# Performance work log

Measured on AMD Instinct MI355X. Metric: run time of the kernel, lower is better.

Reference implementation:

```python
import jax, jax.numpy as jnp
import numpy as np

EPS = 1e-5
D_MODEL, D_INNER, D_STATE, DT_RANK, K = 2048, 4096, 16, 128, 4

def setup_inputs() -> dict:
    key = jax.random.key(0)
    ks = jax.random.split(key, 13)
    B = 128
    s = lambda k, shape, sc=0.02: jax.random.normal(k, shape, jnp.float32) * sc
    return {
        "hidden_states": jax.random.normal(ks[0], (B, 1, D_MODEL), jnp.float32),
        "conv_state": jax.random.normal(ks[1], (B, D_INNER, K - 1), jnp.float32),
        "ssm_state": jax.random.normal(ks[2], (B, D_INNER, D_STATE), jnp.float32),
        "norm_w": jnp.ones((D_MODEL,), jnp.float32),
        "in_proj_w": s(ks[3], (2 * D_INNER, D_MODEL)),           # no bias (HF Mamba default)
        "conv_w": s(ks[4], (D_INNER, K), 0.1),                    # depthwise conv kernel
        "conv_b": s(ks[5], (D_INNER,), 0.1),
        "x_proj_w": s(ks[6], (DT_RANK + 2 * D_STATE, D_INNER)),
        "dt_proj_w": s(ks[7], (D_INNER, DT_RANK)),
        "dt_proj_b": s(ks[8], (D_INNER,), 0.1),
        "A_log": jnp.log(jnp.broadcast_to(jnp.arange(1, D_STATE + 1, dtype=jnp.float32), (D_INNER, D_STATE))),
        "D": jnp.ones((D_INNER,), jnp.float32),
        "out_proj_w": s(ks[9], (D_MODEL, D_INNER)),               # no bias
    }

def reference(hidden_states, conv_state, ssm_state, norm_w, in_proj_w, conv_w, conv_b,
              x_proj_w, dt_proj_w, dt_proj_b, A_log, D, out_proj_w):
    x = hidden_states[:, 0, :]                                   # (B, d_model)
    # RMSNorm (pre-norm)
    normed = x * jax.lax.rsqrt(jnp.mean(x * x, axis=-1, keepdims=True) + EPS) * norm_w
    # in_proj -> gate z and conv branch xc
    xz = normed @ in_proj_w.T                                    # (B, 2*d_inner)
    xc, z = jnp.split(xz, 2, axis=-1)
    # depthwise causal conv, single-step with rolling cache
    conv_in = jnp.concatenate([conv_state, xc[:, :, None]], axis=-1)  # (B, d_inner, K)
    new_conv_state = conv_in[:, :, 1:]
    xact = jax.nn.silu(jnp.sum(conv_in * conv_w[None], axis=-1) + conv_b)  # (B, d_inner)
    # input-dependent SSM params
    proj = xact @ x_proj_w.T                                     # (B, dt_rank + 2*d_state)
    dt_raw = proj[:, :DT_RANK]
    Bmat = proj[:, DT_RANK:DT_RANK + D_STATE]                    # (B, d_state)
    Cmat = proj[:, DT_RANK + D_STATE:]                           # (B, d_state)
    dt = jax.nn.softplus(dt_raw @ dt_proj_w.T + dt_proj_b)       # (B, d_inner)
    A = -jnp.exp(A_log)                                          # (d_inner, d_state)
    dA = jnp.exp(dt[:, :, None] * A[None])                       # (B, d_inner, d_state)
    dB = dt[:, :, None] * Bmat[:, None, :]
    new_ssm_state = ssm_state * dA + dB * xact[:, :, None]
    y = jnp.sum(new_ssm_state * Cmat[:, None, :], axis=-1) + D * xact
    y = y * jax.nn.silu(z)
    out = y @ out_proj_w.T                                       # (B, d_model)
    output = out[:, None, :] + hidden_states                     # residual add
    return output, new_conv_state, new_ssm_state
```

## Files before the change

kernel.cpp:

```cpp
#include <hip/hip_runtime.h>

typedef __attribute__((ext_vector_type(8))) short bf16x8;
typedef __attribute__((ext_vector_type(4))) float f32x4;
typedef __attribute__((ext_vector_type(8))) unsigned short u16x8;
typedef __attribute__((ext_vector_type(4))) unsigned short u16x4;
typedef __attribute__((ext_vector_type(2))) unsigned u32x2;

#define DM 2048
#define DI 4096
#define BATCH 128

__device__ __forceinline__ unsigned short f2bf(float f) {
  union { float f; unsigned u; } v; v.f = f;
  unsigned r = v.u + 0x7FFFu + ((v.u >> 16) & 1u);
  return (unsigned short)(r >> 16);
}
__device__ __forceinline__ float bf2f(unsigned short u) {
  union { unsigned u; float f; } v; v.u = (unsigned)u << 16; return v.f;
}
__device__ __forceinline__ unsigned pk2bf(float lo, float hi) {
  unsigned r;
  asm("v_cvt_pk_bf16_f32 %0, %1, %2" : "=v"(r) : "v"(lo), "v"(hi));
  return r;
}
__device__ __forceinline__ float sigm(float x) { return 1.f / (1.f + __expf(-x)); }

constexpr int BK = 64;
constexpr int LDT = BK + 8;

#define LDREGS(AR, ARF, BR, kb_) do {                                                     \
    int kb = (kb_);                                                                       \
    if constexpr (ABF) {                                                                  \
      _Pragma("unroll") for (int i = 0; i < BM / 32; ++i) {                               \
        int idx = tid + i * 256, r = idx >> 3, c = (idx & 7) * 8;                         \
        AR[i] = *(const u16x8*)&((const unsigned short*)Ag)[(long)(m0 + r) * lda + kb + c]; \
      }                                                                                   \
    } else {                                                                              \
      _Pragma("unroll") for (int i = 0; i < BM / 16; ++i) {                               \
        int idx = tid + i * 256, r = idx >> 4, c = (idx & 15) * 4;                        \
        ARF[i] = *(const f32x4*)&((const float*)Ag)[(long)(m0 + r) * lda + kb + c];       \
      }                                                                                   \
    }                                                                                     \
    _Pragma("unroll") for (int i = 0; i < BN / 16; ++i) {                                 \
      int idx = tid + i * 256, r = idx >> 4, c = (idx & 15) * 4;                          \
      BR[i] = *(const f32x4*)&Bg[(long)(n0 + r) * ldb + kb + c];                          \
    }                                                                                     \
  } while (0)

#define STLDS(AR, ARF, BR, buf_) do {                                                     \
    unsigned short* As_ = lds + (buf_) * BUF;                                             \
    unsigned short* Bs_ = As_ + BM * LDT;                                                 \
    if constexpr (ABF) {                                                                  \
      _Pragma("unroll") for (int i = 0; i < BM / 32; ++i) {                               \
        int idx = tid + i * 256, r = idx >> 3, c = (idx & 7) * 8;                         \
        *(u16x8*)&As_[r * LDT + c] = AR[i];                                               \
      }                                                                                   \
    } else {                                                                              \
      _Pragma("unroll") for (int i = 0; i < BM / 16; ++i) {                               \
        int idx = tid + i * 256, r = idx >> 4, c = (idx & 15) * 4;                        \
        u32x2 o; o[0] = pk2bf(ARF[i][0], ARF[i][1]); o[1] = pk2bf(ARF[i][2], ARF[i][3]); \
        *(u32x2*)&As_[r * LDT + c] = o;                                                   \
      }                                                                                   \
    }                                                                                     \
    _Pragma("unroll") for (int i = 0; i < BN / 16; ++i) {                                 \
      int idx = tid + i * 256, r = idx >> 4, c = (idx & 15) * 4;                          \
      u32x2 o; o[0] = pk2bf(BR[i][0], BR[i][1]); o[1] = pk2bf(BR[i][2], BR[i][3]);       \
      *(u32x2*)&Bs_[r * LDT + c] = o;                                                     \
    }                                                                                     \
  } while (0)

#define COMPUTE(buf_) do {                                                                \
    const unsigned short* As_ = lds + (buf_) * BUF;                                       \
    const unsigned short* Bs_ = As_ + BM * LDT;                                           \
    _Pragma("unroll") for (int kk = 0; kk < BK; kk += 32) {                               \
      int kr = kk + lhi * 8;                                                              \
      bf16x8 af[MI], bfr[NF];                                                             \
      _Pragma("unroll") for (int mi = 0; mi < MI; ++mi)                                   \
        af[mi] = *(const bf16x8*)&As_[(wm * (BM / 2) + mi * 16 + llo) * LDT + kr];        \
      _Pragma("unroll") for (int ni = 0; ni < NF; ++ni)                                   \
        bfr[ni] = *(const bf16x8*)&Bs_[(wn * 16 * NF + ni * 16 + llo) * LDT + kr];        \
      _Pragma("unroll") for (int mi = 0; mi < MI; ++mi)                                   \
        _Pragma("unroll") for (int ni = 0; ni < NF; ++ni)                                 \
          acc[mi * NF + ni] = __builtin_amdgcn_mfma_f32_16x16x32_bf16(                    \
              af[mi], bfr[ni], acc[mi * NF + ni], 0, 0, 0);                               \
    }                                                                                     \
  } while (0)

template<int BM, int BN, bool ABF>
__device__ __forceinline__ void gemmMN(const void* Ag, int lda, const float* Bg, int ldb,
                                       int m0, int n0, int k0, int k1, unsigned short* lds,
                                       f32x4* acc) {
  constexpr int NF = BN / 32;
  constexpr int MI = BM / 32;
  constexpr int BUF = (BM + BN) * LDT;
  const int tid = threadIdx.x, lane = tid & 63, wave = tid >> 6;
  const int wm = wave >> 1, wn = wave & 1, llo = lane & 15, lhi = lane >> 4;

  u16x8 ar0[ABF ? BM / 32 : 1], ar1[ABF ? BM / 32 : 1];
  f32x4 arf0[ABF ? 1 : BM / 16], arf1[ABF ? 1 : BM / 16];
  f32x4 br0[BN / 16], br1[BN / 16];

  const int nt = (k1 - k0) / BK;
  LDREGS(ar0, arf0, br0, k0);
  LDREGS(ar1, arf1, br1, k0 + BK);
  STLDS(ar0, arf0, br0, 0);
  __syncthreads();
  int t = 0;
  while (true) {
    if (t + 2 < nt) LDREGS(ar0, arf0, br0, k0 + (t + 2) * BK);
    COMPUTE(0);
    if (t + 1 < nt) STLDS(ar1, arf1, br1, 1);
    __syncthreads();
    if (++t == nt) break;
    if (t + 2 < nt) LDREGS(ar1, arf1, br1, k0 + (t + 2) * BK);
    COMPUTE(1);
    if (t + 1 < nt) STLDS(ar0, arf0, br0, 0);
    __syncthreads();
    if (++t == nt) break;
  }
}

__global__ __launch_bounds__(256) void k01_prep(const float* __restrict__ hs,
                                                const float* __restrict__ nw,
                                                unsigned short* __restrict__ normed,
                                                float* __restrict__ outp,
                                                float* __restrict__ xz,
                                                float* __restrict__ proj) {
  int blk = blockIdx.x, tid = threadIdx.x;
  int t = blk * 256 + tid;
  f32x4 z = {};
  *(f32x4*)&xz[t * 4] = z;
  if (t < 65536) *(f32x4*)&outp[t * 4] = *(const f32x4*)&hs[t * 4];
  if (t < 5120) *(f32x4*)&proj[t * 4] = z;
  if (blk < 128) {
    int b = blk;
    const float* xr = hs + (long)b * DM;
    f32x4 v0 = *(const f32x4*)&xr[tid * 4];
    f32x4 v1 = *(const f32x4*)&xr[(tid + 256) * 4];
    float ss = v0[0]*v0[0] + v0[1]*v0[1] + v0[2]*v0[2] + v0[3]*v0[3]
             + v1[0]*v1[0] + v1[1]*v1[1] + v1[2]*v1[2] + v1[3]*v1[3];
    for (int off = 32; off; off >>= 1) ss += __shfl_xor(ss, off);
    __shared__ float red[4];
    if ((tid & 63) == 0) red[tid >> 6] = ss;
    __syncthreads();
    ss = red[0] + red[1] + red[2] + red[3];
    float rstd = rsqrtf(ss * (1.f / DM) + 1e-5f);
    f32x4 w0 = *(const f32x4*)&nw[tid * 4];
    f32x4 w1 = *(const f32x4*)&nw[(tid + 256) * 4];
    u32x2 o0, o1;
    o0[0] = pk2bf(v0[0] * rstd * w0[0], v0[1] * rstd * w0[1]);
    o0[1] = pk2bf(v0[2] * rstd * w0[2], v0[3] * rstd * w0[3]);
    o1[0] = pk2bf(v1[0] * rstd * w1[0], v1[1] * rstd * w1[1]);
    o1[1] = pk2bf(v1[2] * rstd * w1[2], v1[3] * rstd * w1[3]);
    *(u32x2*)&normed[(long)b * DM + tid * 4] = o0;
    *(u32x2*)&normed[(long)b * DM + (tid + 256) * 4] = o1;
  }
}

__global__ __launch_bounds__(256) void k2_inproj(const unsigned short* __restrict__ normed,
                                                 const float* __restrict__ W,
                                                 float* __restrict__ xz) {
  __shared__ unsigned short lds[2 * (128 + 64) * LDT];
  f32x4 acc[8] = {};
  int bn = blockIdx.x, sk = blockIdx.y;
  gemmMN<128, 64, true>(normed, DM, W, DM, 0, bn * 64, sk * 512, sk * 512 + 512, lds, acc);
  int tid = threadIdx.x, lane = tid & 63, wave = tid >> 6, wm = wave >> 1, wn = wave & 1;
  int llo = lane & 15, lhi = lane >> 4;
#pragma unroll
  for (int mi = 0; mi < 4; ++mi)
#pragma unroll
    for (int ni = 0; ni < 2; ++ni)
#pragma unroll
      for (int r = 0; r < 4; ++r) {
        int b = wm * 64 + mi * 16 + lhi * 4 + r;
        int n = bn * 64 + wn * 32 + ni * 16 + llo;
        atomicAdd(&xz[(long)b * 8192 + n], acc[mi * 2 + ni][r]);
      }
}

__global__ __launch_bounds__(256) void e2_conv(const float* __restrict__ xz,
                                               const float* __restrict__ conv_state,
                                               const float* __restrict__ conv_w,
                                               const float* __restrict__ conv_b,
                                               float* __restrict__ out_ncs,
                                               float* __restrict__ xact_f,
                                               unsigned short* __restrict__ xact_b,
                                               unsigned short* __restrict__ szb) {
  int p = blockIdx.x * 256 + threadIdx.x;
  int b = p >> 12, n = p & 4095;
  float xc = xz[(long)b * 8192 + n];
  float z  = xz[(long)b * 8192 + DI + n];
  const float* cs = conv_state + (long)p * 3;
  float c0 = cs[0], c1 = cs[1], c2 = cs[2];
  f32x4 cw = *(const f32x4*)&conv_w[n * 4];
  float xs = c0 * cw[0] + c1 * cw[1] + c2 * cw[2] + xc * cw[3] + conv_b[n];
  float xa = xs * sigm(xs);
  float* ncs = out_ncs + (long)p * 3;
  ncs[0] = c1; ncs[1] = c2; ncs[2] = xc;
  xact_f[p] = xa;
  xact_b[p] = f2bf(xa);
  szb[p] = f2bf(z * sigm(z));
}

__global__ __launch_bounds__(256) void k3_xproj(const unsigned short* __restrict__ xact_b,
                                                const float* __restrict__ XW,
                                                float* __restrict__ proj) {
  __shared__ unsigned short lds[2 * (128 + 32) * LDT];
  f32x4 acc[4] = {};
  int bn = blockIdx.x, kc = blockIdx.y;
  gemmMN<128, 32, true>(xact_b, DI, XW, DI, 0, bn * 32, kc * 128, kc * 128 + 128, lds, acc);
  int tid = threadIdx.x, lane = tid & 63, wave = tid >> 6, wm = wave >> 1, wn = wave & 1;
  int llo = lane & 15, lhi = lane >> 4;
  int n = bn * 32 + wn * 16 + llo;
#pragma unroll
  for (int mi = 0; mi < 4; ++mi)
#pragma unroll
    for (int r = 0; r < 4; ++r) {
      int b = wm * 64 + mi * 16 + lhi * 4 + r;
      atomicAdd(&proj[b * 160 + n], acc[mi][r]);
    }
}

__global__ __launch_bounds__(256) void k45_dtssm(const float* __restrict__ proj,
                                                 const float* __restrict__ DW,
                                                 const float* __restrict__ dtb,
                                                 const float* __restrict__ A_log,
                                                 const float* __restrict__ Dp,
                                                 const float* __restrict__ ssm,
                                                 const float* __restrict__ xact_f,
                                                 const unsigned short* __restrict__ szb,
                                                 float* __restrict__ out_nss,
                                                 unsigned short* __restrict__ yz_b) {
  __shared__ unsigned short lds[2 * (32 + 32) * LDT];
  f32x4 acc[1] = {};
  int nb = blockIdx.x, mb = blockIdx.y;
  gemmMN<32, 32, false>(proj, 160, DW, 128, mb * 32, nb * 32, 0, 128, lds, acc);
  int tid = threadIdx.x, lane = tid & 63, wave = tid >> 6, wm = wave >> 1, wn = wave & 1;
  int llo = lane & 15, lhi = lane >> 4;
  int n = nb * 32 + wn * 16 + llo;
  float dtbn = dtb[n], Dn = Dp[n];
  f32x4 Al0 = *(const f32x4*)&A_log[n * 16];
  f32x4 Al1 = *(const f32x4*)&A_log[n * 16 + 4];
  f32x4 Al2 = *(const f32x4*)&A_log[n * 16 + 8];
  f32x4 Al3 = *(const f32x4*)&A_log[n * 16 + 12];
  float aS[16];
#pragma unroll
  for (int j = 0; j < 4; ++j) {
    aS[j] = -__expf(Al0[j]); aS[4 + j] = -__expf(Al1[j]);
    aS[8 + j] = -__expf(Al2[j]); aS[12 + j] = -__expf(Al3[j]);
  }
#pragma unroll
  for (int r = 0; r < 4; ++r) {
    int b = mb * 32 + wm * 16 + lhi * 4 + r;
    long p = (long)b * DI + n;
    float v = acc[0][r] + dtbn;
    float dtv = (v > 20.f) ? v : log1pf(__expf(v));
    float xa = xact_f[p];
    const float* Bp = proj + b * 160 + 128;
    const float* Cp = proj + b * 160 + 144;
    const float* sp = ssm + p * 16;
    float* np = out_nss + p * 16;
    float y = 0.f;
#pragma unroll
    for (int q = 0; q < 4; ++q) {
      f32x4 sv = *(const f32x4*)&sp[q * 4];
      f32x4 Bv = *(const f32x4*)&Bp[q * 4];
      f32x4 Cv = *(const f32x4*)&Cp[q * 4];
      f32x4 nv;
#pragma unroll
      for (int j = 0; j < 4; ++j) {
        float dA = __expf(dtv * aS[q * 4 + j]);
        nv[j] = sv[j] * dA + dtv * Bv[j] * xa;
        y += nv[j] * Cv[j];
      }
      *(f32x4*)&np[q * 4] = nv;
    }
    yz_b[p] = f2bf((y + Dn * xa) * bf2f(szb[p]));
  }
}

__global__ __launch_bounds__(256) void k5_outproj(const unsigned short* __restrict__ yz_b,
                                                  const float* __restrict__ OW,
                                                  float* __restrict__ outp) {
  __shared__ unsigned short lds[2 * (128 + 32) * LDT];
  f32x4 acc[4] = {};
  int bn = blockIdx.x, sk = blockIdx.y;
  gemmMN<128, 32, true>(yz_b, DI, OW, DI, 0, bn * 32, sk * 512, sk * 512 + 512, lds, acc);
  int tid = threadIdx.x, lane = tid & 63, wave = tid >> 6, wm = wave >> 1, wn = wave & 1;
  int llo = lane & 15, lhi = lane >> 4;
  int n = bn * 32 + wn * 16 + llo;
#pragma unroll
  for (int mi = 0; mi < 4; ++mi)
#pragma unroll
    for (int r = 0; r < 4; ++r) {
      int b = wm * 64 + mi * 16 + lhi * 4 + r;
      atomicAdd(&outp[(long)b * DM + n], acc[mi][r]);
    }
}

extern "C" void kernel_launch(void* const* d_in, const int* in_sizes, int n_in, void* d_out,
                              int out_size, void* d_ws, size_t ws_size, hipStream_t stream) {
  const float* hs         = (const float*)d_in[0];
  const float* conv_state = (const float*)d_in[1];
  const float* ssm        = (const float*)d_in[2];
  const float* norm_w     = (const float*)d_in[3];
  const float* in_proj_w  = (const float*)d_in[4];
  const float* conv_w     = (const float*)d_in[5];
  const float* conv_b     = (const float*)d_in[6];
  const float* x_proj_w   = (const float*)d_in[7];
  const float* dt_proj_w  = (const float*)d_in[8];
  const float* dt_proj_b  = (const float*)d_in[9];
  const float* A_log      = (const float*)d_in[10];
  const float* Dp         = (const float*)d_in[11];
  const float* out_proj_w = (const float*)d_in[12];

  float* outp    = (float*)d_out;
  float* out_ncs = outp + 262144;
  float* out_nss = outp + 262144 + 1572864;

  char* ws = (char*)d_ws;
  unsigned short* normed = (unsigned short*)(ws);
  float*          xz     = (float*)(ws + 2097152);
  unsigned short* yz_b   = (unsigned short*)(ws + 2097152);
  float*          xact_f = (float*)(ws + 6291456);
  unsigned short* xact_b = (unsigned short*)(ws + 8388608);
  unsigned short* szb    = (unsigned short*)(ws + 9437184);
  float*          proj   = (float*)(ws + 10485760);

  hipLaunchKernelGGL(k01_prep, dim3(1024), dim3(256), 0, stream, hs, norm_w, normed, outp, xz, proj);
  hipLaunchKernelGGL(k2_inproj, dim3(128, 4), dim3(256), 0, stream, normed, in_proj_w, xz);
  hipLaunchKernelGGL(e2_conv, dim3(2048), dim3(256), 0, stream, xz, conv_state, conv_w, conv_b,
                     out_ncs, xact_f, xact_b, szb);
  hipLaunchKernelGGL(k3_xproj, dim3(5, 32), dim3(256), 0, stream, xact_b, x_proj_w, proj);
  hipLaunchKernelGGL(k45_dtssm, dim3(128, 4), dim3(256), 0, stream, proj, dt_proj_w, dt_proj_b,
                     A_log, Dp, ssm, xact_f, szb, out_nss, yz_b);
  hipLaunchKernelGGL(k5_outproj, dim3(64, 8), dim3(256), 0, stream, yz_b, out_proj_w, outp);
}
```

Baseline: 77.72 us.

## Stream fp32 weights directly into MFMA registers with LDS-resident activation tile

```diff
diff --git a/kernel.cpp b/kernel.cpp
--- a/kernel.cpp
+++ b/kernel.cpp
@@ -5,6 +5,7 @@
 typedef __attribute__((ext_vector_type(8))) unsigned short u16x8;
 typedef __attribute__((ext_vector_type(4))) unsigned short u16x4;
 typedef __attribute__((ext_vector_type(2))) unsigned u32x2;
+typedef __attribute__((ext_vector_type(4))) unsigned u32x4u;
 
 #define DM 2048
 #define DI 4096
@@ -24,6 +25,49 @@
   return r;
 }
 __device__ __forceinline__ float sigm(float x) { return 1.f / (1.f + __expf(-x)); }
+
+__device__ __forceinline__ void stream_gemm(const unsigned short* __restrict__ Ab, long lda,
+                                            const float* __restrict__ Bg, long ldb,
+                                            int n0, int k0, unsigned short* As, f32x4* acc) {
+  const int tid = threadIdx.x, lane = tid & 63, wave = tid >> 6;
+  const int wm = wave >> 1, wn = wave & 1, llo = lane & 15, lhi = lane >> 4;
+#pragma unroll
+  for (int i = 0; i < 32; ++i) {
+    int idx = tid + i * 256;
+    int r = idx >> 6, c8 = (idx & 63) * 8;
+    int kb = c8 * 2;
+    *(u16x8*)&((char*)As)[r * 1024 + (kb ^ ((r & 7) << 4))] =
+        *(const u16x8*)&Ab[(long)r * lda + k0 + c8];
+  }
+  __syncthreads();
+#pragma unroll
+  for (int kk = 0; kk < 512; kk += 32) {
+    bf16x8 af[4], bfr[2];
+#pragma unroll
+    for (int mi = 0; mi < 4; ++mi) {
+      int row = wm * 64 + mi * 16 + llo;
+      int kb = (kk + lhi * 8) * 2;
+      af[mi] = *(const bf16x8*)&((const char*)As)[row * 1024 + (kb ^ ((row & 7) << 4))];
+    }
+#pragma unroll
+    for (int ni = 0; ni < 2; ++ni) {
+      long n = n0 + wn * 32 + ni * 16 + llo;
+      const float* bp = &Bg[n * ldb + k0 + kk + lhi * 8];
+      f32x4 b0 = *(const f32x4*)bp;
+      f32x4 b1 = *(const f32x4*)(bp + 4);
+      union { u32x4u u; bf16x8 h; } cv;
+      cv.u[0] = pk2bf(b0[0], b0[1]); cv.u[1] = pk2bf(b0[2], b0[3]);
+      cv.u[2] = pk2bf(b1[0], b1[1]); cv.u[3] = pk2bf(b1[2], b1[3]);
+      bfr[ni] = cv.h;
+    }
+#pragma unroll
+    for (int mi = 0; mi < 4; ++mi)
+#pragma unroll
+      for (int ni = 0; ni < 2; ++ni)
+        acc[mi * 2 + ni] =
+            __builtin_amdgcn_mfma_f32_16x16x32_bf16(af[mi], bfr[ni], acc[mi * 2 + ni], 0, 0, 0);
+  }
+}
 
 constexpr int BK = 64;
 constexpr int LDT = BK + 8;
@@ -157,13 +201,13 @@
   }
 }
 
-__global__ __launch_bounds__(256) void k2_inproj(const unsigned short* __restrict__ normed,
-                                                 const float* __restrict__ W,
-                                                 float* __restrict__ xz) {
-  __shared__ unsigned short lds[2 * (128 + 64) * LDT];
+__global__ __launch_bounds__(256) void k2s_inproj(const unsigned short* __restrict__ normed,
+                                                  const float* __restrict__ W,
+                                                  float* __restrict__ xz) {
+  __shared__ unsigned short As[128 * 512];
   f32x4 acc[8] = {};
   int bn = blockIdx.x, sk = blockIdx.y;
-  gemmMN<128, 64, true>(normed, DM, W, DM, 0, bn * 64, sk * 512, sk * 512 + 512, lds, acc);
+  stream_gemm(normed, DM, W, DM, bn * 64, sk * 512, As, acc);
   int tid = threadIdx.x, lane = tid & 63, wave = tid >> 6, wm = wave >> 1, wn = wave & 1;
   int llo = lane & 15, lhi = lane >> 4;
 #pragma unroll
@@ -279,23 +323,25 @@
   }
 }
 
-__global__ __launch_bounds__(256) void k5_outproj(const unsigned short* __restrict__ yz_b,
-                                                  const float* __restrict__ OW,
-                                                  float* __restrict__ outp) {
-  __shared__ unsigned short lds[2 * (128 + 32) * LDT];
-  f32x4 acc[4] = {};
+__global__ __launch_bounds__(256) void k5s_outproj(const unsigned short* __restrict__ yz_b,
+                                                   const float* __restrict__ OW,
+                                                   float* __restrict__ outp) {
+  __shared__ unsigned short As[128 * 512];
+  f32x4 acc[8] = {};
   int bn = blockIdx.x, sk = blockIdx.y;
-  gemmMN<128, 32, true>(yz_b, DI, OW, DI, 0, bn * 32, sk * 512, sk * 512 + 512, lds, acc);
+  stream_gemm(yz_b, DI, OW, DI, bn * 64, sk * 512, As, acc);
   int tid = threadIdx.x, lane = tid & 63, wave = tid >> 6, wm = wave >> 1, wn = wave & 1;
   int llo = lane & 15, lhi = lane >> 4;
-  int n = bn * 32 + wn * 16 + llo;
 #pragma unroll
   for (int mi = 0; mi < 4; ++mi)
 #pragma unroll
-    for (int r = 0; r < 4; ++r) {
-      int b = wm * 64 + mi * 16 + lhi * 4 + r;
-      atomicAdd(&outp[(long)b * DM + n], acc[mi][r]);
-    }
+    for (int ni = 0; ni < 2; ++ni)
+#pragma unroll
+      for (int r = 0; r < 4; ++r) {
+        int b = wm * 64 + mi * 16 + lhi * 4 + r;
+        int n = bn * 64 + wn * 32 + ni * 16 + llo;
+        atomicAdd(&outp[(long)b * DM + n], acc[mi * 2 + ni][r]);
+      }
 }
 
 extern "C" void kernel_launch(void* const* d_in, const int* in_sizes, int n_in, void* d_out,
@@ -328,11 +374,11 @@
   float*          proj   = (float*)(ws + 10485760);
 
   hipLaunchKernelGGL(k01_prep, dim3(1024), dim3(256), 0, stream, hs, norm_w, normed, outp, xz, proj);
-  hipLaunchKernelGGL(k2_inproj, dim3(128, 4), dim3(256), 0, stream, normed, in_proj_w, xz);
+  hipLaunchKernelGGL(k2s_inproj, dim3(128, 4), dim3(256), 0, stream, normed, in_proj_w, xz);
   hipLaunchKernelGGL(e2_conv, dim3(2048), dim3(256), 0, stream, xz, conv_state, conv_w, conv_b,
                      out_ncs, xact_f, xact_b, szb);
   hipLaunchKernelGGL(k3_xproj, dim3(5, 32), dim3(256), 0, stream, xact_b, x_proj_w, proj);
   hipLaunchKernelGGL(k45_dtssm, dim3(128, 4), dim3(256), 0, stream, proj, dt_proj_w, dt_proj_b,
                      A_log, Dp, ssm, xact_f, szb, out_nss, yz_b);
-  hipLaunchKernelGGL(k5_outproj, dim3(64, 8), dim3(256), 0, stream, yz_b, out_proj_w, outp);
-}
+  hipLaunchKernelGGL(k5s_outproj, dim3(32, 8), dim3(256), 0, stream, yz_b, out_proj_w, outp);
+}
```

Result: slower. 97.60 us (+25.6%).

## Replace split-K atomic accumulation with partial buffers and explicit reduction passes

Applied to the files above, without the earlier changes.

```diff
diff --git a/kernel.cpp b/kernel.cpp
--- a/kernel.cpp
+++ b/kernel.cpp
@@ -3,7 +3,6 @@
 typedef __attribute__((ext_vector_type(8))) short bf16x8;
 typedef __attribute__((ext_vector_type(4))) float f32x4;
 typedef __attribute__((ext_vector_type(8))) unsigned short u16x8;
-typedef __attribute__((ext_vector_type(4))) unsigned short u16x4;
 typedef __attribute__((ext_vector_type(2))) unsigned u32x2;
 
 #define DM 2048
@@ -120,52 +119,42 @@
   }
 }
 
-__global__ __launch_bounds__(256) void k01_prep(const float* __restrict__ hs,
-                                                const float* __restrict__ nw,
-                                                unsigned short* __restrict__ normed,
-                                                float* __restrict__ outp,
-                                                float* __restrict__ xz,
-                                                float* __restrict__ proj) {
-  int blk = blockIdx.x, tid = threadIdx.x;
-  int t = blk * 256 + tid;
-  f32x4 z = {};
-  *(f32x4*)&xz[t * 4] = z;
-  if (t < 65536) *(f32x4*)&outp[t * 4] = *(const f32x4*)&hs[t * 4];
-  if (t < 5120) *(f32x4*)&proj[t * 4] = z;
-  if (blk < 128) {
-    int b = blk;
-    const float* xr = hs + (long)b * DM;
-    f32x4 v0 = *(const f32x4*)&xr[tid * 4];
-    f32x4 v1 = *(const f32x4*)&xr[(tid + 256) * 4];
-    float ss = v0[0]*v0[0] + v0[1]*v0[1] + v0[2]*v0[2] + v0[3]*v0[3]
-             + v1[0]*v1[0] + v1[1]*v1[1] + v1[2]*v1[2] + v1[3]*v1[3];
-    for (int off = 32; off; off >>= 1) ss += __shfl_xor(ss, off);
-    __shared__ float red[4];
-    if ((tid & 63) == 0) red[tid >> 6] = ss;
-    __syncthreads();
-    ss = red[0] + red[1] + red[2] + red[3];
-    float rstd = rsqrtf(ss * (1.f / DM) + 1e-5f);
-    f32x4 w0 = *(const f32x4*)&nw[tid * 4];
-    f32x4 w1 = *(const f32x4*)&nw[(tid + 256) * 4];
-    u32x2 o0, o1;
-    o0[0] = pk2bf(v0[0] * rstd * w0[0], v0[1] * rstd * w0[1]);
-    o0[1] = pk2bf(v0[2] * rstd * w0[2], v0[3] * rstd * w0[3]);
-    o1[0] = pk2bf(v1[0] * rstd * w1[0], v1[1] * rstd * w1[1]);
-    o1[1] = pk2bf(v1[2] * rstd * w1[2], v1[3] * rstd * w1[3]);
-    *(u32x2*)&normed[(long)b * DM + tid * 4] = o0;
-    *(u32x2*)&normed[(long)b * DM + (tid + 256) * 4] = o1;
-  }
+__global__ __launch_bounds__(256) void k1_rmsnorm(const float* __restrict__ hs,
+                                                  const float* __restrict__ nw,
+                                                  unsigned short* __restrict__ normed) {
+  int b = blockIdx.x, tid = threadIdx.x;
+  const float* xr = hs + (long)b * DM;
+  f32x4 v0 = *(const f32x4*)&xr[tid * 4];
+  f32x4 v1 = *(const f32x4*)&xr[(tid + 256) * 4];
+  float ss = v0[0]*v0[0] + v0[1]*v0[1] + v0[2]*v0[2] + v0[3]*v0[3]
+           + v1[0]*v1[0] + v1[1]*v1[1] + v1[2]*v1[2] + v1[3]*v1[3];
+  for (int off = 32; off; off >>= 1) ss += __shfl_xor(ss, off);
+  __shared__ float red[4];
+  if ((tid & 63) == 0) red[tid >> 6] = ss;
+  __syncthreads();
+  ss = red[0] + red[1] + red[2] + red[3];
+  float rstd = rsqrtf(ss * (1.f / DM) + 1e-5f);
+  f32x4 w0 = *(const f32x4*)&nw[tid * 4];
+  f32x4 w1 = *(const f32x4*)&nw[(tid + 256) * 4];
+  u32x2 o0, o1;
+  o0[0] = pk2bf(v0[0] * rstd * w0[0], v0[1] * rstd * w0[1]);
+  o0[1] = pk2bf(v0[2] * rstd * w0[2], v0[3] * rstd * w0[3]);
+  o1[0] = pk2bf(v1[0] * rstd * w1[0], v1[1] * rstd * w1[1]);
+  o1[1] = pk2bf(v1[2] * rstd * w1[2], v1[3] * rstd * w1[3]);
+  *(u32x2*)&normed[(long)b * DM + tid * 4] = o0;
+  *(u32x2*)&normed[(long)b * DM + (tid + 256) * 4] = o1;
 }
 
 __global__ __launch_bounds__(256) void k2_inproj(const unsigned short* __restrict__ normed,
                                                  const float* __restrict__ W,
-                                                 float* __restrict__ xz) {
+                                                 float* __restrict__ xzp) {
   __shared__ unsigned short lds[2 * (128 + 64) * LDT];
   f32x4 acc[8] = {};
   int bn = blockIdx.x, sk = blockIdx.y;
   gemmMN<128, 64, true>(normed, DM, W, DM, 0, bn * 64, sk * 512, sk * 512 + 512, lds, acc);
   int tid = threadIdx.x, lane = tid & 63, wave = tid >> 6, wm = wave >> 1, wn = wave & 1;
   int llo = lane & 15, lhi = lane >> 4;
+  float* dst = xzp + (long)sk * (BATCH * 8192);
 #pragma unroll
   for (int mi = 0; mi < 4; ++mi)
 #pragma unroll
@@ -174,11 +163,11 @@
       for (int r = 0; r < 4; ++r) {
         int b = wm * 64 + mi * 16 + lhi * 4 + r;
         int n = bn * 64 + wn * 32 + ni * 16 + llo;
-        atomicAdd(&xz[(long)b * 8192 + n], acc[mi * 2 + ni][r]);
+        dst[(long)b * 8192 + n] = acc[mi * 2 + ni][r];
       }
 }
 
-__global__ __launch_bounds__(256) void e2_conv(const float* __restrict__ xz,
+__global__ __launch_bounds__(256) void e2_conv(const float* __restrict__ xzp,
                                                const float* __restrict__ conv_state,
                                                const float* __restrict__ conv_w,
                                                const float* __restrict__ conv_b,
@@ -188,8 +177,13 @@
                                                unsigned short* __restrict__ szb) {
   int p = blockIdx.x * 256 + threadIdx.x;
   int b = p >> 12, n = p & 4095;
-  float xc = xz[(long)b * 8192 + n];
-  float z  = xz[(long)b * 8192 + DI + n];
+  long base = (long)b * 8192 + n;
+  float xc = 0.f, z = 0.f;
+#pragma unroll
+  for (int s = 0; s < 4; ++s) {
+    xc += xzp[(long)s * (BATCH * 8192) + base];
+    z  += xzp[(long)s * (BATCH * 8192) + base + DI];
+  }
   const float* cs = conv_state + (long)p * 3;
   float c0 = cs[0], c1 = cs[1], c2 = cs[2];
   f32x4 cw = *(const f32x4*)&conv_w[n * 4];
@@ -204,7 +198,7 @@
 
 __global__ __launch_bounds__(256) void k3_xproj(const unsigned short* __restrict__ xact_b,
                                                 const float* __restrict__ XW,
-                                                float* __restrict__ proj) {
+                                                float* __restrict__ projp) {
   __shared__ unsigned short lds[2 * (128 + 32) * LDT];
   f32x4 acc[4] = {};
   int bn = blockIdx.x, kc = blockIdx.y;
@@ -212,13 +206,26 @@
   int tid = threadIdx.x, lane = tid & 63, wave = tid >> 6, wm = wave >> 1, wn = wave & 1;
   int llo = lane & 15, lhi = lane >> 4;
   int n = bn * 32 + wn * 16 + llo;
+  float* dst = projp + (long)kc * (BATCH * 160);
 #pragma unroll
   for (int mi = 0; mi < 4; ++mi)
 #pragma unroll
     for (int r = 0; r < 4; ++r) {
       int b = wm * 64 + mi * 16 + lhi * 4 + r;
-      atomicAdd(&proj[b * 160 + n], acc[mi][r]);
+      dst[b * 160 + n] = acc[mi][r];
     }
+}
+
+__global__ __launch_bounds__(256) void k3r_reduce(const float* __restrict__ projp,
+                                                  float* __restrict__ proj) {
+  int t = blockIdx.x * 256 + threadIdx.x;
+  f32x4 s = {};
+#pragma unroll
+  for (int k = 0; k < 32; ++k) {
+    f32x4 v = *(const f32x4*)&projp[(long)k * (BATCH * 160) + t * 4];
+    s[0] += v[0]; s[1] += v[1]; s[2] += v[2]; s[3] += v[3];
+  }
+  *(f32x4*)&proj[t * 4] = s;
 }
 
 __global__ __launch_bounds__(256) void k45_dtssm(const float* __restrict__ proj,
@@ -281,7 +288,7 @@
 
 __global__ __launch_bounds__(256) void k5_outproj(const unsigned short* __restrict__ yz_b,
                                                   const float* __restrict__ OW,
-                                                  float* __restrict__ outp) {
+                                                  float* __restrict__ op) {
   __shared__ unsigned short lds[2 * (128 + 32) * LDT];
   f32x4 acc[4] = {};
   int bn = blockIdx.x, sk = blockIdx.y;
@@ -289,13 +296,27 @@
   int tid = threadIdx.x, lane = tid & 63, wave = tid >> 6, wm = wave >> 1, wn = wave & 1;
   int llo = lane & 15, lhi = lane >> 4;
   int n = bn * 32 + wn * 16 + llo;
+  float* dst = op + (long)sk * (BATCH * DM);
 #pragma unroll
   for (int mi = 0; mi < 4; ++mi)
 #pragma unroll
     for (int r = 0; r < 4; ++r) {
       int b = wm * 64 + mi * 16 + lhi * 4 + r;
-      atomicAdd(&outp[(long)b * DM + n], acc[mi][r]);
+      dst[(long)b * DM + n] = acc[mi][r];
     }
+}
+
+__global__ __launch_bounds__(256) void k7_out(const float* __restrict__ op,
+                                              const float* __restrict__ hs,
+                                              float* __restrict__ outp) {
+  int t = blockIdx.x * 256 + threadIdx.x;
+  f32x4 s = *(const f32x4*)&hs[t * 4];
+#pragma unroll
+  for (int k = 0; k < 8; ++k) {
+    f32x4 v = *(const f32x4*)&op[(long)k * (BATCH * DM) + t * 4];
+    s[0] += v[0]; s[1] += v[1]; s[2] += v[2]; s[3] += v[3];
+  }
+  *(f32x4*)&outp[t * 4] = s;
 }
 
 extern "C" void kernel_launch(void* const* d_in, const int* in_sizes, int n_in, void* d_out,
@@ -320,19 +341,23 @@
 
   char* ws = (char*)d_ws;
   unsigned short* normed = (unsigned short*)(ws);
-  float*          xz     = (float*)(ws + 2097152);
-  unsigned short* yz_b   = (unsigned short*)(ws + 2097152);
-  float*          xact_f = (float*)(ws + 6291456);
-  unsigned short* xact_b = (unsigned short*)(ws + 8388608);
-  unsigned short* szb    = (unsigned short*)(ws + 9437184);
-  float*          proj   = (float*)(ws + 10485760);
-
-  hipLaunchKernelGGL(k01_prep, dim3(1024), dim3(256), 0, stream, hs, norm_w, normed, outp, xz, proj);
-  hipLaunchKernelGGL(k2_inproj, dim3(128, 4), dim3(256), 0, stream, normed, in_proj_w, xz);
-  hipLaunchKernelGGL(e2_conv, dim3(2048), dim3(256), 0, stream, xz, conv_state, conv_w, conv_b,
+  float*          xact_f = (float*)(ws + (1l << 20));
+  unsigned short* xact_b = (unsigned short*)(ws + (3l << 20));
+  unsigned short* szb    = (unsigned short*)(ws + (4l << 20));
+  float*          proj   = (float*)(ws + (5l << 20));
+  float*          projp  = (float*)(ws + (6l << 20));
+  float*          xzp    = (float*)(ws + (9l << 20));
+  float*          op     = (float*)(ws + (25l << 20));
+  unsigned short* yz_b   = (unsigned short*)(ws + (34l << 20));
+
+  hipLaunchKernelGGL(k1_rmsnorm, dim3(128), dim3(256), 0, stream, hs, norm_w, normed);
+  hipLaunchKernelGGL(k2_inproj, dim3(128, 4), dim3(256), 0, stream, normed, in_proj_w, xzp);
+  hipLaunchKernelGGL(e2_conv, dim3(2048), dim3(256), 0, stream, xzp, conv_state, conv_w, conv_b,
                      out_ncs, xact_f, xact_b, szb);
-  hipLaunchKernelGGL(k3_xproj, dim3(5, 32), dim3(256), 0, stream, xact_b, x_proj_w, proj);
+  hipLaunchKernelGGL(k3_xproj, dim3(5, 32), dim3(256), 0, stream, xact_b, x_proj_w, projp);
+  hipLaunchKernelGGL(k3r_reduce, dim3(20), dim3(256), 0, stream, projp, proj);
   hipLaunchKernelGGL(k45_dtssm, dim3(128, 4), dim3(256), 0, stream, proj, dt_proj_w, dt_proj_b,
                      A_log, Dp, ssm, xact_f, szb, out_nss, yz_b);
-  hipLaunchKernelGGL(k5_outproj, dim3(64, 8), dim3(256), 0, stream, yz_b, out_proj_w, outp);
-}
+  hipLaunchKernelGGL(k5_outproj, dim3(64, 8), dim3(256), 0, stream, yz_b, out_proj_w, op);
+  hipLaunchKernelGGL(k7_out, dim3(256), dim3(256), 0, stream, op, hs, outp);
+}
```

New measurement: 77.65 us. Within noise of the previous version (-0.1%).
